# Kernel tuning notes

Hardware: AMD Instinct MI355X
Metric: run time of the kernel (lower is better)

## Reference

```python
import jax, jax.numpy as jnp
import numpy as np

IRE = 1.0 / 400.0

def _stencil(f):
    # f: [B, C, X, Y]; returns (u,v) 5-point stencil fields, each [B, X-2, Y-2]
    m = f[:, :, 1:-1, 1:-1]
    l = f[:, :, :-2, 1:-1]
    r = f[:, :, 2:, 1:-1]
    b = f[:, :, 1:-1, :-2]
    t = f[:, :, 1:-1, 2:]
    return (m[:, 0], m[:, 1], l[:, 0], l[:, 1], r[:, 0], r[:, 1],
            b[:, 0], b[:, 1], t[:, 0], t[:, 1])

def _residuals(um, vm, ul, vl, ur, vr, ub, vb, ut, vt):
    dudx = (ur - ul) * 0.5
    dvdy = (vt - vb) * 0.5
    dudy = (ut - ub) * 0.5
    dvdx = (vr - vl) * 0.5
    du2dx = 0.25 * ((ur + um) ** 2 - (ul + um) ** 2)
    duvdy = 0.25 * ((ut + um) * (vt + vm) - (ub + um) * (vb + vm))
    dv2dy = 0.25 * ((vt + vm) ** 2 - (vb + vm) ** 2)
    dvudx = 0.25 * ((vr + vm) * (ur + um) - (vl + vm) * (ul + um))
    dudx2 = ur - um * 2 + ul
    dudy2 = ut - um * 2 + ub
    dvdx2 = vr - vm * 2 + vl
    dvdy2 = vt - vm * 2 + vb
    mass = dudx + dvdy
    mom_u = du2dx + duvdy - (dudx2 + dudy2) * IRE
    mom_v = dvudx + dv2dy - (dvdx2 + dvdy2) * IRE
    return mass, mom_u, mom_v, dudx, dudy, dvdx, dvdy

def setup_inputs() -> dict:
    key = jax.random.key(0)
    k1, k2 = jax.random.split(key)
    pred = jax.random.normal(k1, (64, 2, 512, 512), dtype=jnp.float32)
    trut = jax.random.normal(k2, (64, 2, 512, 512), dtype=jnp.float32)
    return {"pred": pred, "trut": trut}

def reference(pred, trut):
    mass_t, momu_t, momv_t, dudx_t, dudy_t, dvdx_t, dvdy_t = _residuals(*_stencil(trut))
    mass_p, momu_p, momv_p, dudx_p, dudy_p, dvdx_p, dvdy_p = _residuals(*_stencil(pred))
    lossMass = jnp.mean(jnp.abs(mass_t - mass_p))
    lossMom = jnp.mean(jnp.abs(momu_t - momu_p) + jnp.abs(momv_t - momv_p))
    lossGdl = jnp.mean(jnp.abs(dudx_t - dudx_p) + jnp.abs(dudy_t - dudy_p)
                       + jnp.abs(dvdx_t - dvdx_p) + jnp.abs(dvdy_t - dvdy_p)) / 4.0
    lossL1 = jnp.mean(jnp.abs(pred - trut))
    # lossGdl computed (as in original) but unused in the final combination
    del lossGdl
    return (lossMass * 5 + lossMom * 25 + lossL1) / 3
```

## Files before the change

kernel.cpp:

```cpp
#include <hip/hip_runtime.h>

#define IRE (1.0f / 400.0f)

constexpr int W = 512;
constexpr int H = 512;
constexpr int NB = 64;
constexpr int ROWS = 32;
constexpr int CHUNKS = H / ROWS;
constexpr int STRIPS = 2;

__device__ __forceinline__ void residuals3(
    float um, float vm, float ul, float vl, float ur, float vr,
    float ub, float vb, float ut, float vt,
    float& mass, float& momu, float& momv)
{
    float dudx = (ur - ul) * 0.5f;
    float dvdy = (vt - vb) * 0.5f;
    float ru = ur + um, lu = ul + um, tu_ = ut + um, bu = ub + um;
    float rv = vr + vm, lv = vl + vm, tv_ = vt + vm, bv = vb + vm;
    float du2dx = 0.25f * (ru * ru - lu * lu);
    float duvdy = 0.25f * (tu_ * tv_ - bu * bv);
    float dv2dy = 0.25f * (tv_ * tv_ - bv * bv);
    float dvudx = 0.25f * (rv * ru - lv * lu);
    float dudx2 = ur - 2.0f * um + ul;
    float dudy2 = ut - 2.0f * um + ub;
    float dvdx2 = vr - 2.0f * vm + vl;
    float dvdy2 = vt - 2.0f * vm + vb;
    mass = dudx + dvdy;
    momu = du2dx + duvdy - (dudx2 + dudy2) * IRE;
    momv = dvudx + dv2dy - (dvdx2 + dvdy2) * IRE;
}

__global__ __launch_bounds__(64) void loss_main(
    const float* __restrict__ pred, const float* __restrict__ trut,
    double* __restrict__ acc)
{
    const int lane = threadIdx.x;
    int bid = blockIdx.x;
    const int strip = bid % STRIPS; bid /= STRIPS;
    const int chunk = bid % CHUNKS; bid /= CHUNKS;
    const int b = bid;

    const int r0 = chunk * ROWS;
    const int js = strip * (64 * 4) + lane * 4;

    const size_t CH = (size_t)H * W;
    const float* g_tu = trut + (size_t)b * 2 * CH;
    const float* g_tv = g_tu + CH;
    const float* g_pu = pred + (size_t)b * 2 * CH;
    const float* g_pv = g_pu + CH;

    const int lo = (r0 > 0) ? r0 : 1;
    const int hi = (r0 + ROWS < H - 1) ? (r0 + ROWS) : (H - 1);

    float accMass = 0.0f, accMom = 0.0f, accL1 = 0.0f;

    float4 Ptu, Ptv, Ppu, Ppv;
    float4 Xtu, Xtv, Xpu, Xpv;
    float4 Ntu, Ntv, Npu, Npv;

    auto loadRow = [&](int r, float4& a, float4& bb, float4& c, float4& d) {
        const size_t off = (size_t)r * W + js;
        a  = *(const float4*)(g_tu + off);
        bb = *(const float4*)(g_tv + off);
        c  = *(const float4*)(g_pu + off);
        d  = *(const float4*)(g_pv + off);
        if (r >= r0 && r < r0 + ROWS) {
            accL1 += fabsf(c.x - a.x) + fabsf(c.y - a.y) + fabsf(c.z - a.z) + fabsf(c.w - a.w)
                   + fabsf(d.x - bb.x) + fabsf(d.y - bb.y) + fabsf(d.z - bb.z) + fabsf(d.w - bb.w);
        }
    };

    loadRow(lo - 1, Ptu, Ptv, Ppu, Ppv);
    loadRow(lo,     Xtu, Xtv, Xpu, Xpv);
    loadRow(lo + 1, Ntu, Ntv, Npu, Npv);

    for (int i = lo; i < hi; ++i) {
        float4 Qtu = {0,0,0,0}, Qtv = {0,0,0,0}, Qpu = {0,0,0,0}, Qpv = {0,0,0,0};
        if (i + 2 <= hi) loadRow(i + 2, Qtu, Qtv, Qpu, Qpv);

        float l_tu = __shfl_up(Xtu.w, 1);
        float l_tv = __shfl_up(Xtv.w, 1);
        float l_pu = __shfl_up(Xpu.w, 1);
        float l_pv = __shfl_up(Xpv.w, 1);
        float r_tu = __shfl_down(Xtu.x, 1);
        float r_tv = __shfl_down(Xtv.x, 1);
        float r_pu = __shfl_down(Xpu.x, 1);
        float r_pv = __shfl_down(Xpv.x, 1);
        if (lane == 0 && js > 0) {
            const size_t o = (size_t)i * W + js - 1;
            l_tu = g_tu[o]; l_tv = g_tv[o]; l_pu = g_pu[o]; l_pv = g_pv[o];
        }
        if (lane == 63 && js + 4 < W) {
            const size_t o = (size_t)i * W + js + 4;
            r_tu = g_tu[o]; r_tv = g_tv[o]; r_pu = g_pu[o]; r_pv = g_pv[o];
        }

        const float Ctu[6] = {l_tu, Xtu.x, Xtu.y, Xtu.z, Xtu.w, r_tu};
        const float Ctv[6] = {l_tv, Xtv.x, Xtv.y, Xtv.z, Xtv.w, r_tv};
        const float Cpu[6] = {l_pu, Xpu.x, Xpu.y, Xpu.z, Xpu.w, r_pu};
        const float Cpv[6] = {l_pv, Xpv.x, Xpv.y, Xpv.z, Xpv.w, r_pv};
        const float Pu[4] = {Ptu.x, Ptu.y, Ptu.z, Ptu.w};
        const float Pv[4] = {Ptv.x, Ptv.y, Ptv.z, Ptv.w};
        const float PU[4] = {Ppu.x, Ppu.y, Ppu.z, Ppu.w};
        const float PV[4] = {Ppv.x, Ppv.y, Ppv.z, Ppv.w};
        const float Nu[4] = {Ntu.x, Ntu.y, Ntu.z, Ntu.w};
        const float Nv[4] = {Ntv.x, Ntv.y, Ntv.z, Ntv.w};
        const float NU[4] = {Npu.x, Npu.y, Npu.z, Npu.w};
        const float NV[4] = {Npv.x, Npv.y, Npv.z, Npv.w};

        #pragma unroll
        for (int k = 0; k < 4; ++k) {
            const int j = js + k;
            if (j >= 1 && j <= W - 2) {
                float mT, uT, vT, mP, uP, vP;
                residuals3(Ctu[k+1], Ctv[k+1], Pu[k], Pv[k], Nu[k], Nv[k],
                           Ctu[k],   Ctv[k],   Ctu[k+2], Ctv[k+2], mT, uT, vT);
                residuals3(Cpu[k+1], Cpv[k+1], PU[k], PV[k], NU[k], NV[k],
                           Cpu[k],   Cpv[k],   Cpu[k+2], Cpv[k+2], mP, uP, vP);
                accMass += fabsf(mT - mP);
                accMom  += fabsf(uT - uP) + fabsf(vT - vP);
            }
        }

        Ptu = Xtu; Ptv = Xtv; Ppu = Xpu; Ppv = Xpv;
        Xtu = Ntu; Xtv = Ntv; Xpu = Npu; Xpv = Npv;
        Ntu = Qtu; Ntv = Qtv; Npu = Qpu; Npv = Qpv;
    }

    float res = 5.0f * accMass + 25.0f * accMom;
    float l1  = accL1;
    #pragma unroll
    for (int off = 32; off > 0; off >>= 1) {
        res += __shfl_down(res, off);
        l1  += __shfl_down(l1, off);
    }
    if (lane == 0) {
        atomicAdd(&acc[0], (double)res);
        atomicAdd(&acc[1], (double)l1);
    }
}

__global__ void loss_final(const double* __restrict__ acc, float* __restrict__ out)
{
    const double nRes = 64.0 * 510.0 * 510.0;
    const double nL1  = 64.0 * 2.0 * 512.0 * 512.0;
    out[0] = (float)((acc[0] / nRes + acc[1] / nL1) / 3.0);
}

extern "C" void kernel_launch(void* const* d_in, const int* in_sizes, int n_in,
                              void* d_out, int out_size, void* d_ws, size_t ws_size,
                              hipStream_t stream)
{
    const float* pred = (const float*)d_in[0];
    const float* trut = (const float*)d_in[1];
    double* acc = (double*)d_ws;
    hipMemsetAsync(acc, 0, 2 * sizeof(double), stream);
    const int grid = NB * CHUNKS * STRIPS;
    loss_main<<<grid, 64, 0, stream>>>(pred, trut, acc);
    loss_final<<<1, 1, 0, stream>>>(acc, (float*)d_out);
}
```

Before: 324.2 us.

## Shrink row chunks and replace atomic accumulation with per-block partials

Each block now covers 8 rows instead of 32, which quadruples the grid to give more blocks in flight for latency hiding. It also replaces double-precision global atomics with per-block partial sums that a 256-thread final kernel reduces, and drops the memset. Smaller chunks raise the share of halo rows each block reloads, and the workspace must now hold 2 doubles per block.

After: 297.8 us. -8.1%, faster.

```diff
diff --git a/kernel.cpp b/kernel.cpp
--- a/kernel.cpp
+++ b/kernel.cpp
@@ -5,9 +5,10 @@
 constexpr int W = 512;
 constexpr int H = 512;
 constexpr int NB = 64;
-constexpr int ROWS = 32;
+constexpr int ROWS = 8;
 constexpr int CHUNKS = H / ROWS;
 constexpr int STRIPS = 2;
+constexpr int GRID = NB * CHUNKS * STRIPS;
 
 __device__ __forceinline__ void residuals3(
     float um, float vm, float ul, float vl, float ur, float vr,
@@ -33,7 +34,7 @@
 
 __global__ __launch_bounds__(64) void loss_main(
     const float* __restrict__ pred, const float* __restrict__ trut,
-    double* __restrict__ acc)
+    double* __restrict__ partial)
 {
     const int lane = threadIdx.x;
     int bid = blockIdx.x;
@@ -136,16 +137,36 @@
         l1  += __shfl_down(l1, off);
     }
     if (lane == 0) {
-        atomicAdd(&acc[0], (double)res);
-        atomicAdd(&acc[1], (double)l1);
+        partial[(size_t)blockIdx.x * 2 + 0] = (double)res;
+        partial[(size_t)blockIdx.x * 2 + 1] = (double)l1;
     }
 }
 
-__global__ void loss_final(const double* __restrict__ acc, float* __restrict__ out)
+__global__ __launch_bounds__(256) void loss_final(
+    const double* __restrict__ partial, float* __restrict__ out)
 {
-    const double nRes = 64.0 * 510.0 * 510.0;
-    const double nL1  = 64.0 * 2.0 * 512.0 * 512.0;
-    out[0] = (float)((acc[0] / nRes + acc[1] / nL1) / 3.0);
+    __shared__ double sres[4], sl1[4];
+    const int t = threadIdx.x;
+    double res = 0.0, l1 = 0.0;
+    for (int i = t; i < GRID; i += 256) {
+        res += partial[(size_t)i * 2 + 0];
+        l1  += partial[(size_t)i * 2 + 1];
+    }
+    #pragma unroll
+    for (int off = 32; off > 0; off >>= 1) {
+        res += __shfl_down(res, off);
+        l1  += __shfl_down(l1, off);
+    }
+    const int wave = t >> 6;
+    if ((t & 63) == 0) { sres[wave] = res; sl1[wave] = l1; }
+    __syncthreads();
+    if (t == 0) {
+        res = sres[0] + sres[1] + sres[2] + sres[3];
+        l1  = sl1[0] + sl1[1] + sl1[2] + sl1[3];
+        const double nRes = 64.0 * 510.0 * 510.0;
+        const double nL1  = 64.0 * 2.0 * 512.0 * 512.0;
+        out[0] = (float)((res / nRes + l1 / nL1) / 3.0);
+    }
 }
 
 extern "C" void kernel_launch(void* const* d_in, const int* in_sizes, int n_in,
@@ -154,9 +175,7 @@
 {
     const float* pred = (const float*)d_in[0];
     const float* trut = (const float*)d_in[1];
-    double* acc = (double*)d_ws;
-    hipMemsetAsync(acc, 0, 2 * sizeof(double), stream);
-    const int grid = NB * CHUNKS * STRIPS;
-    loss_main<<<grid, 64, 0, stream>>>(pred, trut, acc);
-    loss_final<<<1, 1, 0, stream>>>(acc, (float*)d_out);
+    double* partial = (double*)d_ws;
+    loss_main<<<GRID, 64, 0, stream>>>(pred, trut, partial);
+    loss_final<<<1, 256, 0, stream>>>(partial, (float*)d_out);
 }
```
